# Kernel tuning notes

Hardware: AMD Instinct MI355X
Metric: run time of the kernel (lower is better)

Reference implementation:

```python
import jax, jax.numpy as jnp
import numpy as np

B, H, T, D = 4, 16, 2048, 64


def setup_inputs() -> dict:
    key = jax.random.key(0)
    kq, kk, kv = jax.random.split(key, 3)
    q = jax.random.normal(kq, (B, H, T, D), dtype=jnp.float32)
    k = jax.random.normal(kk, (B, H, T, D), dtype=jnp.float32)
    v = jax.random.normal(kv, (B, H, T, D), dtype=jnp.float32)
    return {"q": q, "k": k, "v": v}


def reference(q, k, v):
    # scores: [B,H,T,T] = q @ k^T (no softmax, linear attention)
    scores = jnp.einsum("bhtd,bhsd->bhts", q, k)
    # causal multiplicative mask: lower-triangular ones (zero out future keys)
    t = q.shape[-2]
    causal = jnp.tril(jnp.ones((t, t), dtype=scores.dtype))  # [T,T]
    scores = scores * causal  # broadcast over [B,H]
    # output: [B,H,T,D] = masked_scores @ v
    return jnp.einsum("bhts,bhsd->bhtd", scores, v)
```

## Files before the change

kernel.cpp:

```cpp
#include <hip/hip_runtime.h>
#include <hip/hip_bf16.h>


#define B_   4
#define H_   16
#define T_   2048
#define D_   64
#define BH_  64
#define CCH  256
#define NCH  8
#define LPAD 8
#define LW   (D_ + LPAD)

typedef __bf16 bf16x8 __attribute__((ext_vector_type(8)));
typedef float  f32x4  __attribute__((ext_vector_type(4)));


__global__ __launch_bounds__(256) void kv_chunk_kernel(
    const float* __restrict__ k, const float* __restrict__ v,
    float* __restrict__ kvws) {
  __shared__ __align__(16) __bf16 KT[D_][LW];
  __shared__ __align__(16) __bf16 VT[D_][LW];

  const int tid  = threadIdx.x;
  const int lane = tid & 63;
  const int w    = tid >> 6;
  const int quad = lane >> 4;
  const int l15  = lane & 15;
  const int bh   = blockIdx.x >> 3;
  const int c    = blockIdx.x & (NCH - 1);
  const long base = ((long)bh * T_ + (long)c * CCH) * D_;

  const f32x4 vzero = {0.f, 0.f, 0.f, 0.f};
  f32x4 acc[4];
#pragma unroll
  for (int n = 0; n < 4; ++n) acc[n] = vzero;

  const int sl = tid >> 2;
  const int d0 = (tid & 3) * 16;

  for (int st = 0; st < 4; ++st) {
    __syncthreads();
    {
      const float* krow = k + base + (long)(st * 64 + sl) * D_ + d0;
      const float* vrow = v + base + (long)(st * 64 + sl) * D_ + d0;
#pragma unroll
      for (int x4 = 0; x4 < 4; ++x4) {
        float4 kx = *(const float4*)(krow + x4 * 4);
        float4 vx = *(const float4*)(vrow + x4 * 4);
        int dd = d0 + x4 * 4;
        KT[dd + 0][sl] = (__bf16)kx.x;
        KT[dd + 1][sl] = (__bf16)kx.y;
        KT[dd + 2][sl] = (__bf16)kx.z;
        KT[dd + 3][sl] = (__bf16)kx.w;
        VT[dd + 0][sl] = (__bf16)vx.x;
        VT[dd + 1][sl] = (__bf16)vx.y;
        VT[dd + 2][sl] = (__bf16)vx.z;
        VT[dd + 3][sl] = (__bf16)vx.w;
      }
    }
    __syncthreads();
#pragma unroll
    for (int ks = 0; ks < 2; ++ks) {
      bf16x8 a = *(const bf16x8*)&KT[w * 16 + l15][ks * 32 + quad * 8];
#pragma unroll
      for (int n = 0; n < 4; ++n) {
        bf16x8 b = *(const bf16x8*)&VT[n * 16 + l15][ks * 32 + quad * 8];
        acc[n] = __builtin_amdgcn_mfma_f32_16x16x32_bf16(a, b, acc[n], 0, 0, 0);
      }
    }
  }
  float* out = kvws + ((long)blockIdx.x << 12);
#pragma unroll
  for (int n = 0; n < 4; ++n)
#pragma unroll
    for (int rr = 0; rr < 4; ++rr)
      out[(w * 16 + quad * 4 + rr) * 64 + n * 16 + l15] = acc[n][rr];
}

__global__ __launch_bounds__(256) void attn_chunk_kernel(
    const float* __restrict__ q, const float* __restrict__ k,
    const float* __restrict__ v, const float* __restrict__ kvws,
    float* __restrict__ out) {
  __shared__ __align__(16) __bf16 KVT[D_][LW];
  __shared__ __align__(16) __bf16 Kj[64][LW];
  __shared__ __align__(16) __bf16 VTj[D_][LW];
  __shared__ __align__(16) __bf16 Sw[4][16][LW];

  const int tid  = threadIdx.x;
  const int lane = tid & 63;
  const int w    = tid >> 6;
  const int quad = lane >> 4;
  const int l15  = lane & 15;
  const int bh   = blockIdx.x >> 3;
  const int c    = blockIdx.x & (NCH - 1);
  const long base = ((long)bh * T_ + (long)c * CCH) * D_;

  float kvacc[16];
#pragma unroll
  for (int i = 0; i < 16; ++i) kvacc[i] = 0.f;
  const float* wsbh = kvws + ((long)(bh * NCH) << 12);
  for (int cc = 0; cc < c; ++cc) {
    const float* p = wsbh + ((long)cc << 12) + tid;
#pragma unroll
    for (int i = 0; i < 16; ++i) kvacc[i] += p[i << 8];
  }
#pragma unroll
  for (int i = 0; i < 16; ++i) {
    int lin = tid + (i << 8);
    int d1 = lin >> 6, d2 = lin & 63;
    KVT[d2][d1] = (__bf16)kvacc[i];
  }

  bf16x8 qf[4][2];
#pragma unroll
  for (int i = 0; i < 4; ++i) {
    int row = (w + 4 * i) * 16 + l15;
    const float* qp = q + base + (long)row * D_ + quad * 8;
#pragma unroll
    for (int ks = 0; ks < 2; ++ks) {
      float4 lo = *(const float4*)(qp + ks * 32);
      float4 hi = *(const float4*)(qp + ks * 32 + 4);
      bf16x8 f;
      f[0] = (__bf16)lo.x; f[1] = (__bf16)lo.y;
      f[2] = (__bf16)lo.z; f[3] = (__bf16)lo.w;
      f[4] = (__bf16)hi.x; f[5] = (__bf16)hi.y;
      f[6] = (__bf16)hi.z; f[7] = (__bf16)hi.w;
      qf[i][ks] = f;
    }
  }

  const f32x4 vzero = {0.f, 0.f, 0.f, 0.f};
  f32x4 acc[4][4];
#pragma unroll
  for (int i = 0; i < 4; ++i)
#pragma unroll
    for (int n = 0; n < 4; ++n) acc[i][n] = vzero;

  __syncthreads();

#pragma unroll
  for (int ks = 0; ks < 2; ++ks)
#pragma unroll
    for (int n = 0; n < 4; ++n) {
      bf16x8 b = *(const bf16x8*)&KVT[n * 16 + l15][ks * 32 + quad * 8];
#pragma unroll
      for (int i = 0; i < 4; ++i)
        acc[i][n] =
            __builtin_amdgcn_mfma_f32_16x16x32_bf16(qf[i][ks], b, acc[i][n], 0, 0, 0);
    }

  const int sl = tid >> 2;
  const int d0 = (tid & 3) * 16;
  for (int j = 0; j < 4; ++j) {
    __syncthreads();
    {
      const float* krow = k + base + (long)(j * 64 + sl) * D_ + d0;
      const float* vrow = v + base + (long)(j * 64 + sl) * D_ + d0;
#pragma unroll
      for (int x4 = 0; x4 < 4; ++x4) {
        float4 kx = *(const float4*)(krow + x4 * 4);
        float4 vx = *(const float4*)(vrow + x4 * 4);
        int dd = d0 + x4 * 4;
        Kj[sl][dd + 0] = (__bf16)kx.x;
        Kj[sl][dd + 1] = (__bf16)kx.y;
        Kj[sl][dd + 2] = (__bf16)kx.z;
        Kj[sl][dd + 3] = (__bf16)kx.w;
        VTj[dd + 0][sl] = (__bf16)vx.x;
        VTj[dd + 1][sl] = (__bf16)vx.y;
        VTj[dd + 2][sl] = (__bf16)vx.z;
        VTj[dd + 3][sl] = (__bf16)vx.w;
      }
    }
    __syncthreads();
    for (int i = j; i < 4; ++i) {
      f32x4 s[4];
#pragma unroll
      for (int n = 0; n < 4; ++n) s[n] = vzero;
#pragma unroll
      for (int ks = 0; ks < 2; ++ks) {
#pragma unroll
        for (int n = 0; n < 4; ++n) {
          bf16x8 b = *(const bf16x8*)&Kj[n * 16 + l15][ks * 32 + quad * 8];
          s[n] = __builtin_amdgcn_mfma_f32_16x16x32_bf16(qf[i][ks], b, s[n], 0, 0, 0);
        }
      }
      __syncthreads();
#pragma unroll
      for (int n = 0; n < 4; ++n) {
#pragma unroll
        for (int rr = 0; rr < 4; ++rr) {
          float val = s[n][rr];
          if (i == j) {
            if (n * 16 + l15 > 16 * w + quad * 4 + rr) val = 0.f;
          }
          Sw[w][quad * 4 + rr][n * 16 + l15] = (__bf16)val;
        }
      }
      __syncthreads();
#pragma unroll
      for (int ks = 0; ks < 2; ++ks) {
        bf16x8 a = *(const bf16x8*)&Sw[w][l15][ks * 32 + quad * 8];
#pragma unroll
        for (int n = 0; n < 4; ++n) {
          bf16x8 b = *(const bf16x8*)&VTj[n * 16 + l15][ks * 32 + quad * 8];
          acc[i][n] =
              __builtin_amdgcn_mfma_f32_16x16x32_bf16(a, b, acc[i][n], 0, 0, 0);
        }
      }
    }
  }

  float* op = out + base;
#pragma unroll
  for (int i = 0; i < 4; ++i) {
    int row = (w + 4 * i) * 16 + quad * 4;
#pragma unroll
    for (int n = 0; n < 4; ++n)
#pragma unroll
      for (int rr = 0; rr < 4; ++rr)
        op[(long)(row + rr) * D_ + n * 16 + l15] = acc[i][n][rr];
  }
}

extern "C" void kernel_launch(void* const* d_in, const int* in_sizes, int n_in,
                              void* d_out, int out_size, void* d_ws, size_t ws_size,
                              hipStream_t stream) {
  const float* q = (const float*)d_in[0];
  const float* k = (const float*)d_in[1];
  const float* v = (const float*)d_in[2];
  float* out = (float*)d_out;
  float* kvws = (float*)d_ws;

  hipLaunchKernelGGL(kv_chunk_kernel, dim3(BH_ * NCH), dim3(256), 0, stream,
                     k, v, kvws);
  hipLaunchKernelGGL(attn_chunk_kernel, dim3(BH_ * NCH), dim3(256), 0, stream,
                     q, k, v, kvws, out);
}
```

Before: 151.7 us.

## Streamline chunked linear attention: fewer barriers, vectorized LDS stores, skip last chunk state

Drops the two block-wide barriers around the per-warp score scratch, since each warp only uses its own Sw slice. Loads of the first K/V sub-tile are hoisted out of the loop and overlapped with the prefix-state reduction. K and the state matrix are packed into LDS with 16-byte bf16x8 stores, and V fragments are kept in registers across the inner loop. The state kernel skips the last chunk, whose state is never read, and launch bounds request two blocks per CU. Removing the warp barriers relies on each warp touching only its own Sw rows; the write-then-read within a warp still needs correct LDS ordering.

```diff
diff --git a/kernel.cpp b/kernel.cpp
--- a/kernel.cpp
+++ b/kernel.cpp
@@ -2,25 +2,98 @@
 #include <hip/hip_bf16.h>
 
 
-#define B_   4
-#define H_   16
 #define T_   2048
 #define D_   64
-#define BH_  64
 #define CCH  256
 #define NCH  8
-#define LPAD 8
-#define LW   (D_ + LPAD)
+#define LW   72
 
 typedef __bf16 bf16x8 __attribute__((ext_vector_type(8)));
 typedef float  f32x4  __attribute__((ext_vector_type(4)));
 
 
-__global__ __launch_bounds__(256) void kv_chunk_kernel(
+__device__ inline bf16x8 pack8(float4 a, float4 b) {
+  bf16x8 r;
+  r[0] = (__bf16)a.x; r[1] = (__bf16)a.y; r[2] = (__bf16)a.z; r[3] = (__bf16)a.w;
+  r[4] = (__bf16)b.x; r[5] = (__bf16)b.y; r[6] = (__bf16)b.z; r[7] = (__bf16)b.w;
+  return r;
+}
+
+__global__ __launch_bounds__(256, 2) void state_kernel(
     const float* __restrict__ k, const float* __restrict__ v,
     float* __restrict__ kvws) {
-  __shared__ __align__(16) __bf16 KT[D_][LW];
-  __shared__ __align__(16) __bf16 VT[D_][LW];
+  __shared__ __align__(16) __bf16 KT[64][LW];
+  __shared__ __align__(16) __bf16 VT[64][LW];
+
+  const int tid  = threadIdx.x;
+  const int lane = tid & 63;
+  const int w    = tid >> 6;
+  const int quad = lane >> 4;
+  const int l15  = lane & 15;
+  const int bh   = blockIdx.x >> 3;
+  const int c    = blockIdx.x & (NCH - 1);
+  if (c == NCH - 1) return;
+  const long base = ((long)bh * T_ + (long)c * CCH) * D_;
+  const int d0   = w * 16;
+
+  const f32x4 vzero = {0.f, 0.f, 0.f, 0.f};
+  f32x4 st[4];
+#pragma unroll
+  for (int n = 0; n < 4; ++n) st[n] = vzero;
+
+  for (int j = 0; j < 4; ++j) {
+    if (j) __syncthreads();
+    {
+      const float* krow = k + base + (long)(j * 64 + lane) * D_ + d0;
+      const float* vrow = v + base + (long)(j * 64 + lane) * D_ + d0;
+      float4 k0 = *(const float4*)(krow + 0),  k1 = *(const float4*)(krow + 4);
+      float4 k2 = *(const float4*)(krow + 8),  k3 = *(const float4*)(krow + 12);
+      float4 v0 = *(const float4*)(vrow + 0),  v1 = *(const float4*)(vrow + 4);
+      float4 v2 = *(const float4*)(vrow + 8),  v3 = *(const float4*)(vrow + 12);
+      KT[d0 +  0][lane] = (__bf16)k0.x; KT[d0 +  1][lane] = (__bf16)k0.y;
+      KT[d0 +  2][lane] = (__bf16)k0.z; KT[d0 +  3][lane] = (__bf16)k0.w;
+      KT[d0 +  4][lane] = (__bf16)k1.x; KT[d0 +  5][lane] = (__bf16)k1.y;
+      KT[d0 +  6][lane] = (__bf16)k1.z; KT[d0 +  7][lane] = (__bf16)k1.w;
+      KT[d0 +  8][lane] = (__bf16)k2.x; KT[d0 +  9][lane] = (__bf16)k2.y;
+      KT[d0 + 10][lane] = (__bf16)k2.z; KT[d0 + 11][lane] = (__bf16)k2.w;
+      KT[d0 + 12][lane] = (__bf16)k3.x; KT[d0 + 13][lane] = (__bf16)k3.y;
+      KT[d0 + 14][lane] = (__bf16)k3.z; KT[d0 + 15][lane] = (__bf16)k3.w;
+      VT[d0 +  0][lane] = (__bf16)v0.x; VT[d0 +  1][lane] = (__bf16)v0.y;
+      VT[d0 +  2][lane] = (__bf16)v0.z; VT[d0 +  3][lane] = (__bf16)v0.w;
+      VT[d0 +  4][lane] = (__bf16)v1.x; VT[d0 +  5][lane] = (__bf16)v1.y;
+      VT[d0 +  6][lane] = (__bf16)v1.z; VT[d0 +  7][lane] = (__bf16)v1.w;
+      VT[d0 +  8][lane] = (__bf16)v2.x; VT[d0 +  9][lane] = (__bf16)v2.y;
+      VT[d0 + 10][lane] = (__bf16)v2.z; VT[d0 + 11][lane] = (__bf16)v2.w;
+      VT[d0 + 12][lane] = (__bf16)v3.x; VT[d0 + 13][lane] = (__bf16)v3.y;
+      VT[d0 + 14][lane] = (__bf16)v3.z; VT[d0 + 15][lane] = (__bf16)v3.w;
+    }
+    __syncthreads();
+    bf16x8 ka0 = *(const bf16x8*)&KT[d0 + l15][quad * 8];
+    bf16x8 ka1 = *(const bf16x8*)&KT[d0 + l15][32 + quad * 8];
+#pragma unroll
+    for (int n = 0; n < 4; ++n) {
+      bf16x8 b0 = *(const bf16x8*)&VT[n * 16 + l15][quad * 8];
+      bf16x8 b1 = *(const bf16x8*)&VT[n * 16 + l15][32 + quad * 8];
+      st[n] = __builtin_amdgcn_mfma_f32_16x16x32_bf16(ka0, b0, st[n], 0, 0, 0);
+      st[n] = __builtin_amdgcn_mfma_f32_16x16x32_bf16(ka1, b1, st[n], 0, 0, 0);
+    }
+  }
+  float* wsp = kvws + ((long)blockIdx.x << 12);
+#pragma unroll
+  for (int n = 0; n < 4; ++n)
+#pragma unroll
+    for (int rr = 0; rr < 4; ++rr)
+      wsp[(d0 + quad * 4 + rr) * 64 + n * 16 + l15] = st[n][rr];
+}
+
+__global__ __launch_bounds__(256, 2) void attn_kernel(
+    const float* __restrict__ q, const float* __restrict__ k,
+    const float* __restrict__ v, const float* __restrict__ kvws,
+    float* __restrict__ out) {
+  __shared__ __align__(16) __bf16 Kj[64][LW];
+  __shared__ __align__(16) __bf16 VT[64][LW];
+  __shared__ __align__(16) __bf16 KVT[64][LW];
+  __shared__ __align__(16) __bf16 Sw[4][16][LW];
 
   const int tid  = threadIdx.x;
   const int lane = tid & 63;
@@ -30,104 +103,55 @@
   const int bh   = blockIdx.x >> 3;
   const int c    = blockIdx.x & (NCH - 1);
   const long base = ((long)bh * T_ + (long)c * CCH) * D_;
-
-  const f32x4 vzero = {0.f, 0.f, 0.f, 0.f};
-  f32x4 acc[4];
-#pragma unroll
-  for (int n = 0; n < 4; ++n) acc[n] = vzero;
-
-  const int sl = tid >> 2;
-  const int d0 = (tid & 3) * 16;
-
-  for (int st = 0; st < 4; ++st) {
-    __syncthreads();
-    {
-      const float* krow = k + base + (long)(st * 64 + sl) * D_ + d0;
-      const float* vrow = v + base + (long)(st * 64 + sl) * D_ + d0;
-#pragma unroll
-      for (int x4 = 0; x4 < 4; ++x4) {
-        float4 kx = *(const float4*)(krow + x4 * 4);
-        float4 vx = *(const float4*)(vrow + x4 * 4);
-        int dd = d0 + x4 * 4;
-        KT[dd + 0][sl] = (__bf16)kx.x;
-        KT[dd + 1][sl] = (__bf16)kx.y;
-        KT[dd + 2][sl] = (__bf16)kx.z;
-        KT[dd + 3][sl] = (__bf16)kx.w;
-        VT[dd + 0][sl] = (__bf16)vx.x;
-        VT[dd + 1][sl] = (__bf16)vx.y;
-        VT[dd + 2][sl] = (__bf16)vx.z;
-        VT[dd + 3][sl] = (__bf16)vx.w;
-      }
-    }
-    __syncthreads();
-#pragma unroll
-    for (int ks = 0; ks < 2; ++ks) {
-      bf16x8 a = *(const bf16x8*)&KT[w * 16 + l15][ks * 32 + quad * 8];
-#pragma unroll
-      for (int n = 0; n < 4; ++n) {
-        bf16x8 b = *(const bf16x8*)&VT[n * 16 + l15][ks * 32 + quad * 8];
-        acc[n] = __builtin_amdgcn_mfma_f32_16x16x32_bf16(a, b, acc[n], 0, 0, 0);
-      }
-    }
-  }
-  float* out = kvws + ((long)blockIdx.x << 12);
-#pragma unroll
-  for (int n = 0; n < 4; ++n)
-#pragma unroll
-    for (int rr = 0; rr < 4; ++rr)
-      out[(w * 16 + quad * 4 + rr) * 64 + n * 16 + l15] = acc[n][rr];
-}
-
-__global__ __launch_bounds__(256) void attn_chunk_kernel(
-    const float* __restrict__ q, const float* __restrict__ k,
-    const float* __restrict__ v, const float* __restrict__ kvws,
-    float* __restrict__ out) {
-  __shared__ __align__(16) __bf16 KVT[D_][LW];
-  __shared__ __align__(16) __bf16 Kj[64][LW];
-  __shared__ __align__(16) __bf16 VTj[D_][LW];
-  __shared__ __align__(16) __bf16 Sw[4][16][LW];
-
-  const int tid  = threadIdx.x;
-  const int lane = tid & 63;
-  const int w    = tid >> 6;
-  const int quad = lane >> 4;
-  const int l15  = lane & 15;
-  const int bh   = blockIdx.x >> 3;
-  const int c    = blockIdx.x & (NCH - 1);
-  const long base = ((long)bh * T_ + (long)c * CCH) * D_;
+  const int d0   = w * 16;
+
+  bf16x8 qf[4][2];
+#pragma unroll
+  for (int i = 0; i < 4; ++i) {
+    const float* qp = q + base + (long)((w + 4 * i) * 16 + l15) * D_ + quad * 8;
+#pragma unroll
+    for (int ks = 0; ks < 2; ++ks)
+      qf[i][ks] = pack8(*(const float4*)(qp + ks * 32),
+                        *(const float4*)(qp + ks * 32 + 4));
+  }
 
   float kvacc[16];
 #pragma unroll
   for (int i = 0; i < 16; ++i) kvacc[i] = 0.f;
-  const float* wsbh = kvws + ((long)(bh * NCH) << 12);
-  for (int cc = 0; cc < c; ++cc) {
-    const float* p = wsbh + ((long)cc << 12) + tid;
-#pragma unroll
-    for (int i = 0; i < 16; ++i) kvacc[i] += p[i << 8];
-  }
-#pragma unroll
-  for (int i = 0; i < 16; ++i) {
-    int lin = tid + (i << 8);
-    int d1 = lin >> 6, d2 = lin & 63;
-    KVT[d2][d1] = (__bf16)kvacc[i];
-  }
-
-  bf16x8 qf[4][2];
-#pragma unroll
-  for (int i = 0; i < 4; ++i) {
-    int row = (w + 4 * i) * 16 + l15;
-    const float* qp = q + base + (long)row * D_ + quad * 8;
-#pragma unroll
-    for (int ks = 0; ks < 2; ++ks) {
-      float4 lo = *(const float4*)(qp + ks * 32);
-      float4 hi = *(const float4*)(qp + ks * 32 + 4);
-      bf16x8 f;
-      f[0] = (__bf16)lo.x; f[1] = (__bf16)lo.y;
-      f[2] = (__bf16)lo.z; f[3] = (__bf16)lo.w;
-      f[4] = (__bf16)hi.x; f[5] = (__bf16)hi.y;
-      f[6] = (__bf16)hi.z; f[7] = (__bf16)hi.w;
-      qf[i][ks] = f;
-    }
+  {
+    const float* wsbh = kvws + ((long)(bh * NCH) << 12);
+    for (int cc = 0; cc < c; ++cc) {
+      const float* p = wsbh + ((long)cc << 12) + d0 * 64 + lane;
+#pragma unroll
+      for (int i = 0; i < 16; ++i) kvacc[i] += p[i * 64];
+    }
+  }
+
+  {
+    const float* krow = k + base + (long)lane * D_ + d0;
+    const float* vrow = v + base + (long)lane * D_ + d0;
+    float4 k0 = *(const float4*)(krow + 0),  k1 = *(const float4*)(krow + 4);
+    float4 k2 = *(const float4*)(krow + 8),  k3 = *(const float4*)(krow + 12);
+    float4 v0 = *(const float4*)(vrow + 0),  v1 = *(const float4*)(vrow + 4);
+    float4 v2 = *(const float4*)(vrow + 8),  v3 = *(const float4*)(vrow + 12);
+    *(bf16x8*)&Kj[lane][d0]     = pack8(k0, k1);
+    *(bf16x8*)&Kj[lane][d0 + 8] = pack8(k2, k3);
+    VT[d0 +  0][lane] = (__bf16)v0.x; VT[d0 +  1][lane] = (__bf16)v0.y;
+    VT[d0 +  2][lane] = (__bf16)v0.z; VT[d0 +  3][lane] = (__bf16)v0.w;
+    VT[d0 +  4][lane] = (__bf16)v1.x; VT[d0 +  5][lane] = (__bf16)v1.y;
+    VT[d0 +  6][lane] = (__bf16)v1.z; VT[d0 +  7][lane] = (__bf16)v1.w;
+    VT[d0 +  8][lane] = (__bf16)v2.x; VT[d0 +  9][lane] = (__bf16)v2.y;
+    VT[d0 + 10][lane] = (__bf16)v2.z; VT[d0 + 11][lane] = (__bf16)v2.w;
+    VT[d0 + 12][lane] = (__bf16)v3.x; VT[d0 + 13][lane] = (__bf16)v3.y;
+    VT[d0 + 14][lane] = (__bf16)v3.z; VT[d0 + 15][lane] = (__bf16)v3.w;
+  }
+  {
+    float4 a0 = {kvacc[0], kvacc[1], kvacc[2], kvacc[3]};
+    float4 a1 = {kvacc[4], kvacc[5], kvacc[6], kvacc[7]};
+    float4 a2 = {kvacc[8], kvacc[9], kvacc[10], kvacc[11]};
+    float4 a3 = {kvacc[12], kvacc[13], kvacc[14], kvacc[15]};
+    *(bf16x8*)&KVT[lane][d0]     = pack8(a0, a1);
+    *(bf16x8*)&KVT[lane][d0 + 8] = pack8(a2, a3);
   }
 
   const f32x4 vzero = {0.f, 0.f, 0.f, 0.f};
@@ -150,63 +174,60 @@
             __builtin_amdgcn_mfma_f32_16x16x32_bf16(qf[i][ks], b, acc[i][n], 0, 0, 0);
     }
 
-  const int sl = tid >> 2;
-  const int d0 = (tid & 3) * 16;
   for (int j = 0; j < 4; ++j) {
-    __syncthreads();
-    {
-      const float* krow = k + base + (long)(j * 64 + sl) * D_ + d0;
-      const float* vrow = v + base + (long)(j * 64 + sl) * D_ + d0;
-#pragma unroll
-      for (int x4 = 0; x4 < 4; ++x4) {
-        float4 kx = *(const float4*)(krow + x4 * 4);
-        float4 vx = *(const float4*)(vrow + x4 * 4);
-        int dd = d0 + x4 * 4;
-        Kj[sl][dd + 0] = (__bf16)kx.x;
-        Kj[sl][dd + 1] = (__bf16)kx.y;
-        Kj[sl][dd + 2] = (__bf16)kx.z;
-        Kj[sl][dd + 3] = (__bf16)kx.w;
-        VTj[dd + 0][sl] = (__bf16)vx.x;
-        VTj[dd + 1][sl] = (__bf16)vx.y;
-        VTj[dd + 2][sl] = (__bf16)vx.z;
-        VTj[dd + 3][sl] = (__bf16)vx.w;
-      }
-    }
-    __syncthreads();
+    if (j) {
+      __syncthreads();
+      const float* krow = k + base + (long)(j * 64 + lane) * D_ + d0;
+      const float* vrow = v + base + (long)(j * 64 + lane) * D_ + d0;
+      float4 k0 = *(const float4*)(krow + 0),  k1 = *(const float4*)(krow + 4);
+      float4 k2 = *(const float4*)(krow + 8),  k3 = *(const float4*)(krow + 12);
+      float4 v0 = *(const float4*)(vrow + 0),  v1 = *(const float4*)(vrow + 4);
+      float4 v2 = *(const float4*)(vrow + 8),  v3 = *(const float4*)(vrow + 12);
+      *(bf16x8*)&Kj[lane][d0]     = pack8(k0, k1);
+      *(bf16x8*)&Kj[lane][d0 + 8] = pack8(k2, k3);
+      VT[d0 +  0][lane] = (__bf16)v0.x; VT[d0 +  1][lane] = (__bf16)v0.y;
+      VT[d0 +  2][lane] = (__bf16)v0.z; VT[d0 +  3][lane] = (__bf16)v0.w;
+      VT[d0 +  4][lane] = (__bf16)v1.x; VT[d0 +  5][lane] = (__bf16)v1.y;
+      VT[d0 +  6][lane] = (__bf16)v1.z; VT[d0 +  7][lane] = (__bf16)v1.w;
+      VT[d0 +  8][lane] = (__bf16)v2.x; VT[d0 +  9][lane] = (__bf16)v2.y;
+      VT[d0 + 10][lane] = (__bf16)v2.z; VT[d0 + 11][lane] = (__bf16)v2.w;
+      VT[d0 + 12][lane] = (__bf16)v3.x; VT[d0 + 13][lane] = (__bf16)v3.y;
+      VT[d0 + 14][lane] = (__bf16)v3.z; VT[d0 + 15][lane] = (__bf16)v3.w;
+      __syncthreads();
+    }
+
+    bf16x8 vb[2][4];
+#pragma unroll
+    for (int ks = 0; ks < 2; ++ks)
+#pragma unroll
+      for (int n = 0; n < 4; ++n)
+        vb[ks][n] = *(const bf16x8*)&VT[n * 16 + l15][ks * 32 + quad * 8];
+
     for (int i = j; i < 4; ++i) {
-      f32x4 s[4];
-#pragma unroll
-      for (int n = 0; n < 4; ++n) s[n] = vzero;
-#pragma unroll
-      for (int ks = 0; ks < 2; ++ks) {
+      f32x4 s4[4];
+#pragma unroll
+      for (int n = 0; n < 4; ++n) s4[n] = vzero;
+#pragma unroll
+      for (int ks = 0; ks < 2; ++ks)
 #pragma unroll
         for (int n = 0; n < 4; ++n) {
           bf16x8 b = *(const bf16x8*)&Kj[n * 16 + l15][ks * 32 + quad * 8];
-          s[n] = __builtin_amdgcn_mfma_f32_16x16x32_bf16(qf[i][ks], b, s[n], 0, 0, 0);
+          s4[n] = __builtin_amdgcn_mfma_f32_16x16x32_bf16(qf[i][ks], b, s4[n], 0, 0, 0);
         }
-      }
-      __syncthreads();
-#pragma unroll
-      for (int n = 0; n < 4; ++n) {
+#pragma unroll
+      for (int n = 0; n < 4; ++n)
 #pragma unroll
         for (int rr = 0; rr < 4; ++rr) {
-          float val = s[n][rr];
-          if (i == j) {
-            if (n * 16 + l15 > 16 * w + quad * 4 + rr) val = 0.f;
-          }
+          float val = s4[n][rr];
+          if (i == j && (n * 16 + l15 > 16 * w + quad * 4 + rr)) val = 0.f;
           Sw[w][quad * 4 + rr][n * 16 + l15] = (__bf16)val;
         }
-      }
-      __syncthreads();
-#pragma unroll
-      for (int ks = 0; ks < 2; ++ks) {
-        bf16x8 a = *(const bf16x8*)&Sw[w][l15][ks * 32 + quad * 8];
-#pragma unroll
-        for (int n = 0; n < 4; ++n) {
-          bf16x8 b = *(const bf16x8*)&VTj[n * 16 + l15][ks * 32 + quad * 8];
-          acc[i][n] =
-              __builtin_amdgcn_mfma_f32_16x16x32_bf16(a, b, acc[i][n], 0, 0, 0);
-        }
+      bf16x8 a0 = *(const bf16x8*)&Sw[w][l15][quad * 8];
+      bf16x8 a1 = *(const bf16x8*)&Sw[w][l15][32 + quad * 8];
+#pragma unroll
+      for (int n = 0; n < 4; ++n) {
+        acc[i][n] = __builtin_amdgcn_mfma_f32_16x16x32_bf16(a0, vb[0][n], acc[i][n], 0, 0, 0);
+        acc[i][n] = __builtin_amdgcn_mfma_f32_16x16x32_bf16(a1, vb[1][n], acc[i][n], 0, 0, 0);
       }
     }
   }
@@ -232,8 +253,7 @@
   float* out = (float*)d_out;
   float* kvws = (float*)d_ws;
 
-  hipLaunchKernelGGL(kv_chunk_kernel, dim3(BH_ * NCH), dim3(256), 0, stream,
-                     k, v, kvws);
-  hipLaunchKernelGGL(attn_chunk_kernel, dim3(BH_ * NCH), dim3(256), 0, stream,
+  hipLaunchKernelGGL(state_kernel, dim3(512), dim3(256), 0, stream, k, v, kvws);
+  hipLaunchKernelGGL(attn_kernel, dim3(512), dim3(256), 0, stream,
                      q, k, v, kvws, out);
 }
```

Result: slower. 162.8 us (+7.4%).
